# Kernel optimization log

Hardware: AMD Instinct MI355X
Metric: run time of the kernel (lower is better)

Reference implementation:

```python
import jax, jax.numpy as jnp
import numpy as np

B, L, D, H, N, F_, DM = 16, 2048, 128, 4, 4, 129, 16
DK = D // H
DFF = 2 * D
INT = int(np.sqrt(D))  # 11
V = F_ + 1


def _uinit(key, shape, fan):
    s = float(np.sqrt(6.0 / fan))
    return jax.random.uniform(key, shape, jnp.float32, -s, s)


def setup_inputs() -> dict:
    key = jax.random.key(0)
    ks = jax.random.split(key, 24)
    return {
        "values": jax.random.normal(ks[0], (B, L), jnp.float32),
        "times": jax.random.uniform(ks[1], (B, L), jnp.float32),
        "variables": jax.random.randint(ks[2], (B, L), 0, F_),
        "input_mask": jax.random.randint(ks[3], (B, L), 0, 2).astype(bool),
        "demographics": jax.random.normal(ks[4], (B, DM), jnp.float32),
        # CVE time
        "W1t": _uinit(ks[5], (1, INT), 1 + INT), "b1t": jnp.zeros((INT,), jnp.float32),
        "W2t": _uinit(ks[6], (INT, D), INT + D),
        # CVE value
        "W1v": _uinit(ks[7], (1, INT), 1 + INT), "b1v": jnp.zeros((INT,), jnp.float32),
        "W2v": _uinit(ks[8], (INT, D), INT + D),
        # variable embedding table
        "var_table": jax.random.normal(ks[9], (V, D), jnp.float32),
        # transformer stacks (init_proj: uniform(-s, s), s = sqrt(6/(fan_in+fan_out)) of last two dims)
        "Wq": _uinit(ks[10], (N, H, D, DK), D + DK),
        "Wk": _uinit(ks[11], (N, H, D, DK), D + DK),
        "Wv": _uinit(ks[12], (N, H, D, DK), D + DK),
        "Wo": _uinit(ks[13], (N, D, D), 2 * D),
        "W1": _uinit(ks[14], (N, D, DFF), D + DFF), "b1": jnp.zeros((N, 1, 1, DFF), jnp.float32),
        "W2": _uinit(ks[15], (N, DFF, D), DFF + D), "b2": jnp.zeros((N, 1, 1, D), jnp.float32),
        # fusion attention
        "Wf": _uinit(ks[16], (D, D), 2 * D), "bf": jnp.zeros((D,), jnp.float32),
        "uf": _uinit(ks[17], (D, 1), D + 1),
        # demographics MLP
        "Wd1": _uinit(ks[18], (DM, 2 * D), DM + 2 * D), "bd1": jnp.zeros((2 * D,), jnp.float32),
        "Wd2": _uinit(ks[19], (2 * D, D), 3 * D), "bd2": jnp.zeros((D,), jnp.float32),
        # head: forecast_fc
        "Wh": _uinit(ks[20], (2 * D, F_), 2 * D + F_), "bh": jnp.zeros((F_,), jnp.float32),
    }


def reference(values, times, variables, input_mask, demographics,
              W1t, b1t, W2t, W1v, b1v, W2v, var_table,
              Wq, Wk, Wv, Wo, W1, b1, W2, b2,
              Wf, bf, uf, Wd1, bd1, Wd2, bd2, Wh, bh):
    FMIN = jnp.finfo(values.dtype).min
    # demographics MLP
    demo = jnp.tanh(demographics @ Wd1 + bd1) @ Wd2 + bd2
    # continuous value embeddings (CVE): x -> tanh(x*W1 + b1) @ W2
    te = jnp.tanh(times[..., None] * W1t[0] + b1t) @ W2t    # [B,L,D]
    ve = jnp.tanh(values[..., None] * W1v[0] + b1v) @ W2v   # [B,L,D]
    x = te + ve + var_table[variables]                      # [B,L,D]
    # additive pairwise mask (finite FMIN, matches torch finfo.min semantics)
    m = input_mask
    pair = m[:, :, None] & m[:, None, :]                    # [B,L,L]
    addm = jnp.where(pair[:, None, :, :], 0.0, FMIN)        # [B,1,L,L]
    n_layers = Wq.shape[0]
    bsz, max_len, _ = x.shape
    for i in range(n_layers):
        q = jnp.einsum('bld,hde->bhle', x, Wq[i])
        k = jnp.einsum('bld,hde->bhle', x, Wk[i])
        v = jnp.einsum('bld,hde->bhle', x, Wv[i])
        A = jnp.einsum('bhle,bhke->bhlk', q, k) + addm      # NOTE: no 1/sqrt(dk) scaling, as in source
        A = jax.nn.softmax(A, axis=-1)
        o = jnp.einsum('bhlk,bhke->blhe', A, v).reshape(bsz, max_len, -1)
        x = o @ Wo[i] + x
        f = jax.nn.gelu(x @ W1[i] + b1[i], approximate=False)
        x = f @ W2[i] + b2[i] + x
    # fusion attention pooling
    att = (jnp.tanh(x @ Wf + bf) @ uf)[:, :, 0]             # [B,L]
    att = att + jnp.where(m, 0.0, FMIN)
    w = jax.nn.softmax(att, axis=-1)
    ts = jnp.sum(x * w[:, :, None], axis=1)                 # [B,D]
    emb = jnp.concatenate([ts, demo], axis=-1)              # [B,2D]
    return emb @ Wh + bh                                    # [B,features_num]
```

## Files before the change

kernel.cpp:

```cpp
#include <hip/hip_runtime.h>
#include <hip/hip_bf16.h>
#include <math.h>

#define B_   16
#define L_   2048
#define D_   128
#define H_   4
#define NL_  4
#define DK_  32
#define DFF_ 256
#define INTD_ 11
#define F_OUT 129
#define DM_  16
#define FMINV (-3.402823466e38f)
#define LOG2E 1.4426950408889634f

#define BL_  (B_*L_)
#define SZ_X (BL_*D_)

#define WT_Q 0
#define WT_K 16384
#define WT_V 32768
#define WT_O 49152
#define WT_1 65536
#define WT_2 98304
#define WT_TOT 131072

typedef __attribute__((ext_vector_type(8))) short bf16x8;
typedef __attribute__((ext_vector_type(4))) float f32x4;

#if __has_builtin(__builtin_amdgcn_exp2f)
#define EXP2F(x) __builtin_amdgcn_exp2f(x)
#else
#define EXP2F(x) __expf(0.69314718055994531f*(x))
#endif

static __device__ __forceinline__ short f2bf(float x) {
    union { __hip_bfloat16 h; short s; } u;
    u.h = __float2bfloat16(x);
    return u.s;
}
static __device__ __forceinline__ float bf2f(short s) {
    union { __hip_bfloat16 h; short t; } u;
    u.t = s;
    return __bfloat162float(u.h);
}
static __device__ __forceinline__ void split2(float v, short& h, short& l) {
    h = f2bf(v); l = f2bf(v - bf2f(h));
}
static __device__ __forceinline__ void split_trunc(float v, short& h, short& l) {
    unsigned u = __float_as_uint(v);
    h = (short)(u >> 16);
    float r = v - __uint_as_float(u & 0xffff0000u);
    l = (short)(__float_as_uint(r) >> 16);
}
static __device__ __forceinline__ void bar_lgkm() {
    asm volatile("s_waitcnt lgkmcnt(0)" ::: "memory");
    __builtin_amdgcn_s_barrier();
}
static __device__ __forceinline__ int find_b(const int* __restrict__ tp, int bidx) {
    int b = 0;
    while (bidx >= tp[b+1]) ++b;
    return b;
}

__global__ __launch_bounds__(256)
void compact_kernel(const int* __restrict__ mask, int* __restrict__ pos,
                    int* __restrict__ kcount, float* __restrict__ cfm,
                    float* __restrict__ x)
{
    int b = blockIdx.x, t = threadIdx.x;
    int lane = t & 63, w = t >> 6;
    __shared__ int wsum[4];
    __shared__ int tot_s;
    int mv[8], loc[8], s = 0;
#pragma unroll
    for (int i = 0; i < 8; ++i) {
        mv[i] = mask[b*L_ + t*8 + i];
        loc[i] = s;
        s += mv[i];
    }
    int v = s;
#pragma unroll
    for (int d = 1; d < 64; d <<= 1) {
        int y = __shfl_up(v, d);
        if (lane >= d) v += y;
    }
    int excl = v - s;
    if (lane == 63) wsum[w] = v;
    __syncthreads();
    int wbase = 0;
    for (int i = 0; i < w; ++i) wbase += wsum[i];
    int base = wbase + excl;
#pragma unroll
    for (int i = 0; i < 8; ++i)
        pos[b*L_ + t*8 + i] = mv[i] ? (base + loc[i]) : -1;
    if (t == 255) { kcount[b] = base + s; tot_s = base + s; }
    __syncthreads();
    int tot = tot_s;
    for (int l = t; l < L_; l += 256) cfm[b*L_ + l] = (l < tot) ? 0.0f : FMINV;
    int end = (tot + 63) & ~63;
    int nz = (end - tot) * D_;
    for (int i = t; i < nz; i += 256)
        x[((size_t)(b*2048 + tot))*D_ + i] = 0.0f;
}

__global__ __launch_bounds__(64)
void tile_prefix_kernel(const int* __restrict__ kcount, int* __restrict__ tprefix)
{
    if (threadIdx.x == 0) {
        int s = 0;
        for (int b = 0; b < B_; ++b) {
            tprefix[b] = s;
            s += (kcount[b] + 63) >> 6;
        }
        tprefix[B_] = s;
    }
}

__global__ __launch_bounds__(128)
void embed_kernel(const float* __restrict__ values, const float* __restrict__ times,
                  const int* __restrict__ variables, const int* __restrict__ pos,
                  const float* __restrict__ W1t, const float* __restrict__ b1t,
                  const float* __restrict__ W2t,
                  const float* __restrict__ W1v, const float* __restrict__ b1v,
                  const float* __restrict__ W2v,
                  const float* __restrict__ var_table, float* __restrict__ x)
{
    int bl = blockIdx.x;
    int p  = pos[bl];
    if (p < 0) return;
    int t  = threadIdx.x;
    __shared__ float th[INTD_], vh[INTD_];
    if (t < INTD_)                th[t]    = tanhf(times[bl]  * W1t[t]    + b1t[t]);
    if (t >= 64 && t < 64+INTD_)  vh[t-64] = tanhf(values[bl] * W1v[t-64] + b1v[t-64]);
    __syncthreads();
    int var = variables[bl];
    float acc = var_table[var*D_ + t];
#pragma unroll
    for (int i = 0; i < INTD_; ++i)
        acc += th[i]*W2t[i*D_ + t] + vh[i]*W2v[i*D_ + t];
    x[((size_t)((bl >> 11)*2048 + p))*D_ + t] = acc;
}

__global__ __launch_bounds__(256)
void split_all_kernel(const float* __restrict__ Wq, const float* __restrict__ Wk,
                      const float* __restrict__ Wv, const float* __restrict__ Wo,
                      const float* __restrict__ W1, const float* __restrict__ W2,
                      const float* __restrict__ Wf,
                      short* __restrict__ hi, short* __restrict__ lo)
{
    int gidx = blockIdx.x*256 + threadIdx.x;
    float v;
    if (gidx < NL_*131072) {
        int layer = gidx >> 17;
        int idx   = gidx & 131071;
        if (idx < 49152) {
            int which = idx >> 14;
            int r = idx & 16383;
            int col = r >> 7, k = r & 127;
            int h = col >> 5, e = col & 31;
            const float* src = ((which == 0) ? Wq : (which == 1) ? Wk : Wv)
                               + (size_t)layer*H_*D_*DK_;
            v = src[(h*D_ + k)*DK_ + e];
        } else if (idx < 65536) {
            int r = idx - 49152;
            int col = r >> 7, k = r & 127;
            v = Wo[(size_t)layer*D_*D_ + k*D_ + col];
        } else if (idx < 98304) {
            int r = idx - 65536;
            int col = r >> 7, k = r & 127;
            v = W1[(size_t)layer*D_*DFF_ + k*DFF_ + col];
        } else {
            int r = idx - 98304;
            int col = r >> 8, k = r & 255;
            v = W2[(size_t)layer*DFF_*D_ + k*D_ + col];
        }
    } else {
        int r = gidx - NL_*131072;
        int col = r >> 7, k = r & 127;
        v = Wf[k*D_ + col];
    }
    short h2, l2; split2(v, h2, l2);
    hi[gidx] = h2; lo[gidx] = l2;
}

__global__ __launch_bounds__(256)
void gemm_qkv_fused(const float* __restrict__ A, const short* __restrict__ Whi,
                    const short* __restrict__ Wlo, const int* __restrict__ tprefix,
                    float* __restrict__ qout,
                    short* __restrict__ khi, short* __restrict__ klo,
                    short* __restrict__ vhiT, short* __restrict__ vloT)
{
    const int bidx = blockIdx.x;
    if (bidx >= tprefix[B_]) return;
    const int bb = find_b(tprefix, bidx);
    const int row0 = bb*2048 + (bidx - tprefix[bb])*64;
    const int sec = blockIdx.y;

    __shared__ short Ahi[64*136];
    __shared__ short Alo[64*136];
    const int t = threadIdx.x;
    const int w = t >> 6, lane = t & 63;
    const int m = lane & 15, qd = lane >> 4;

#pragma unroll
    for (int i = 0; i < 8; ++i) {
        int r = (t >> 5) + 8*i;
        int c = (t & 31) * 4;
        float4 av = *(const float4*)(A + (size_t)(row0 + r)*D_ + c);
        short4 hi4, lo4;
        split2(av.x, hi4.x, lo4.x);
        split2(av.y, hi4.y, lo4.y);
        split2(av.z, hi4.z, lo4.z);
        split2(av.w, hi4.w, lo4.w);
        *(short4*)&Ahi[r*136 + c] = hi4;
        *(short4*)&Alo[r*136 + c] = lo4;
    }
    __syncthreads();

    const short* Wh = Whi + sec*16384;
    const short* Wl = Wlo + sec*16384;
    f32x4 acc[4][2];
#pragma unroll
    for (int r4 = 0; r4 < 4; ++r4)
#pragma unroll
        for (int j = 0; j < 2; ++j) acc[r4][j] = (f32x4){0,0,0,0};

#pragma unroll
    for (int ks = 0; ks < 4; ++ks) {
        bf16x8 wh[2], wl[2];
#pragma unroll
        for (int j = 0; j < 2; ++j) {
            size_t wi = (size_t)(32*w + 16*j + m)*D_ + 32*ks + 8*qd;
            wh[j] = *(const bf16x8*)(Wh + wi);
            wl[j] = *(const bf16x8*)(Wl + wi);
        }
#pragma unroll
        for (int r4 = 0; r4 < 4; ++r4) {
            bf16x8 ah = *(const bf16x8*)&Ahi[(16*r4 + m)*136 + 32*ks + 8*qd];
            bf16x8 al = *(const bf16x8*)&Alo[(16*r4 + m)*136 + 32*ks + 8*qd];
#pragma unroll
            for (int j = 0; j < 2; ++j) {
                acc[r4][j] = __builtin_amdgcn_mfma_f32_16x16x32_bf16(wh[j], ah, acc[r4][j], 0, 0, 0);
                acc[r4][j] = __builtin_amdgcn_mfma_f32_16x16x32_bf16(wh[j], al, acc[r4][j], 0, 0, 0);
                acc[r4][j] = __builtin_amdgcn_mfma_f32_16x16x32_bf16(wl[j], ah, acc[r4][j], 0, 0, 0);
            }
        }
    }

#pragma unroll
    for (int r4 = 0; r4 < 4; ++r4) {
        int row = row0 + 16*r4 + m;
        int l = row & 2047;
#pragma unroll
        for (int j = 0; j < 2; ++j) {
            int col = 32*w + 16*j + 4*qd;
            f32x4 v = acc[r4][j];
            if (sec == 0) {
                float4 sv = {v[0], v[1], v[2], v[3]};
                *(float4*)(qout + (size_t)row*D_ + col) = sv;
            } else if (sec == 1) {
                size_t idx = ((size_t)((bb*4 + w)*2048 + l))*32 + (col & 31);
                short4 hi4, lo4;
                split2(v[0], hi4.x, lo4.x);
                split2(v[1], hi4.y, lo4.y);
                split2(v[2], hi4.z, lo4.z);
                split2(v[3], hi4.w, lo4.w);
                *(short4*)(khi + idx) = hi4;
                *(short4*)(klo + idx) = lo4;
            } else {
                size_t basep = (size_t)(bb*4 + w)*32;
#pragma unroll
                for (int e = 0; e < 4; ++e) {
                    int d = 16*j + 4*qd + e;
                    short hh, ll; split2(v[e], hh, ll);
                    vhiT[(basep + d)*2048 + l] = hh;
                    vloT[(basep + d)*2048 + l] = ll;
                }
            }
        }
    }
}

__global__ __launch_bounds__(256)
void attn_mfma_kernel(const float* __restrict__ q,
                      const short* __restrict__ khi, const short* __restrict__ klo,
                      const short* __restrict__ vhiT, const short* __restrict__ vloT,
                      const int* __restrict__ kcount, const int* __restrict__ tprefix,
                      float* __restrict__ opart, float* __restrict__ mlm,
                      float* __restrict__ mll)
{
    __shared__ short KhiS[2][2048];
    __shared__ short KloS[2][2048];
    __shared__ short Vthi[2][2048];
    __shared__ short Vtlo[2][2048];
    __shared__ short Ps[4][1024];

    const int bidx = blockIdx.x;
    if (bidx >= tprefix[B_]) return;
    const int b  = find_b(tprefix, bidx);
    const int qt = bidx - tprefix[b];
    const int h = blockIdx.y & 3, half = blockIdx.y >> 2;

    const int t    = threadIdx.x;
    const int w    = t >> 6;
    const int lane = t & 63;
    const int m    = lane & 15;
    const int qd   = lane >> 4;

    const int Kb = kcount[b];
    const int nt = (Kb + 63) >> 6;
    const int ntH = (nt + 1) >> 1;
    const int kt0 = half * ntH;
    const int kt1 = (kt0 + ntH < nt) ? (kt0 + ntH) : nt;
    const size_t mlbase = (((size_t)(b*4 + h))*2 + half)*2048;

    if (kt0 >= kt1) {
        if (lane < 16) {
            mlm[mlbase + qt*64 + 16*w + lane] = FMINV;
            mll[mlbase + qt*64 + 16*w + lane] = 0.0f;
        }
        return;
    }

    const size_t hd = ((size_t)(b*4 + h))*2048*32;
    const int vd = t >> 3;
    const int vk = t & 7;
    const size_t vbase = ((size_t)(b*4 + h)*32 + vd)*2048 + vk*8;
    const int vw_off = vd*64 + ((vk ^ (vd & 7)) << 3);

    const int qrow = qt*64 + 16*w + m;
    const float* qp = q + ((size_t)(b*L_ + qrow))*D_ + h*DK_ + 8*qd;
    float qf[8];
    *(float4*)&qf[0] = *(const float4*)qp;
    *(float4*)&qf[4] = *(const float4*)(qp + 4);
    bf16x8 qhi, qlo;
#pragma unroll
    for (int j = 0; j < 8; ++j) {
        float qs = qf[j] * LOG2E;
        short hs = f2bf(qs);
        qhi[j] = hs;
        qlo[j] = f2bf(qs - bf2f(hs));
    }

    bf16x8 pkh, pkl, pvh, pvl;
    {
        const size_t gk = hd + (size_t)kt0*64*32 + t*8;
        pkh = *(const bf16x8*)(khi + gk);
        pkl = *(const bf16x8*)(klo + gk);
        pvh = *(const bf16x8*)(vhiT + vbase + (size_t)kt0*64);
        pvl = *(const bf16x8*)(vloT + vbase + (size_t)kt0*64);
    }

    float m_old = -INFINITY, l_run = 0.0f;
    f32x4 o_acc[2] = {{0,0,0,0},{0,0,0,0}};

    for (int kt = kt0; kt < kt1; ++kt) {
        const int buf = kt & 1;
        *(bf16x8*)&KhiS[buf][t*8] = pkh;
        *(bf16x8*)&KloS[buf][t*8] = pkl;
        *(bf16x8*)&Vthi[buf][vw_off] = pvh;
        *(bf16x8*)&Vtlo[buf][vw_off] = pvl;
        if (kt + 1 < kt1) {
            const size_t gk = hd + (size_t)(kt+1)*64*32 + t*8;
            pkh = *(const bf16x8*)(khi + gk);
            pkl = *(const bf16x8*)(klo + gk);
            pvh = *(const bf16x8*)(vhiT + vbase + (size_t)(kt+1)*64);
            pvl = *(const bf16x8*)(vloT + vbase + (size_t)(kt+1)*64);
        }
        bar_lgkm();
        __builtin_amdgcn_sched_barrier(0);

        f32x4 sf[4];
#pragma unroll
        for (int k4 = 0; k4 < 4; ++k4) {
            bf16x8 ka = *(const bf16x8*)&KhiS[buf][(16*k4 + m)*32 + 8*qd];
            bf16x8 kl = *(const bf16x8*)&KloS[buf][(16*k4 + m)*32 + 8*qd];
            f32x4 c = {0,0,0,0};
            c = __builtin_amdgcn_mfma_f32_16x16x32_bf16(ka, qhi, c, 0, 0, 0);
            c = __builtin_amdgcn_mfma_f32_16x16x32_bf16(ka, qlo, c, 0, 0, 0);
            c = __builtin_amdgcn_mfma_f32_16x16x32_bf16(kl, qhi, c, 0, 0, 0);
            sf[k4] = c;
        }

        float sv[16];
        if (kt == nt - 1) {
            const int rel = Kb - kt*64;
#pragma unroll
            for (int k4 = 0; k4 < 4; ++k4)
#pragma unroll
                for (int e = 0; e < 4; ++e)
                    sv[4*k4+e] = sf[k4][e] +
                        (((16*k4 + 4*qd + e) < rel) ? 0.0f : FMINV);
        } else {
#pragma unroll
            for (int k4 = 0; k4 < 4; ++k4)
#pragma unroll
                for (int e = 0; e < 4; ++e)
                    sv[4*k4+e] = sf[k4][e];
        }

        float mx8[8];
#pragma unroll
        for (int j = 0; j < 8; ++j) mx8[j] = fmaxf(sv[2*j], sv[2*j+1]);
#pragma unroll
        for (int j = 0; j < 4; ++j) mx8[j] = fmaxf(mx8[j], mx8[j+4]);
        float tmax = fmaxf(fmaxf(mx8[0], mx8[1]), fmaxf(mx8[2], mx8[3]));
        tmax = fmaxf(tmax, __shfl_xor(tmax, 16));
        tmax = fmaxf(tmax, __shfl_xor(tmax, 32));
        float mnew  = fmaxf(m_old, tmax);
        float alpha = EXP2F(m_old - mnew);
        float pj[16];
        short pbh[16], pbl[16];
#pragma unroll
        for (int j = 0; j < 16; ++j) {
            float p = EXP2F(sv[j] - mnew);
            pj[j] = p;
            split_trunc(p, pbh[j], pbl[j]);
        }
        float ps8[8];
#pragma unroll
        for (int j = 0; j < 8; ++j) ps8[j] = pj[2*j] + pj[2*j+1];
#pragma unroll
        for (int j = 0; j < 4; ++j) ps8[j] = ps8[j] + ps8[j+4];
        float psum = (ps8[0] + ps8[1]) + (ps8[2] + ps8[3]);
        psum += __shfl_xor(psum, 16);
        psum += __shfl_xor(psum, 32);
        l_run = l_run * alpha + psum;
        m_old = mnew;

#pragma unroll
        for (int k4 = 0; k4 < 4; ++k4) {
            short4 s4h;
            s4h.x = pbh[4*k4+0]; s4h.y = pbh[4*k4+1]; s4h.z = pbh[4*k4+2]; s4h.w = pbh[4*k4+3];
            int chunk = 2*k4 + (qd >> 1);
            int po = m*64 + ((chunk ^ (m & 7)) << 3) + ((qd & 1) << 2);
            *(short4*)&Ps[w][po] = s4h;
        }

        {
            float a0 = __shfl(alpha, 4*qd + 0);
            float a1 = __shfl(alpha, 4*qd + 1);
            float a2 = __shfl(alpha, 4*qd + 2);
            float a3 = __shfl(alpha, 4*qd + 3);
            o_acc[0][0]*=a0; o_acc[0][1]*=a1; o_acc[0][2]*=a2; o_acc[0][3]*=a3;
            o_acc[1][0]*=a0; o_acc[1][1]*=a1; o_acc[1][2]*=a2; o_acc[1][3]*=a3;
        }
#pragma unroll
        for (int s = 0; s < 2; ++s) {
#pragma unroll
            for (int tp = 0; tp < 2; ++tp) {
                bf16x8 pah = *(const bf16x8*)&Ps[w][m*64 + (((4*s + qd) ^ (m & 7)) << 3)];
                int vr = (16*tp + m)*64 + (((4*s + qd) ^ (m & 7)) << 3);
                bf16x8 vh = *(const bf16x8*)&Vthi[buf][vr];
                bf16x8 vl = *(const bf16x8*)&Vtlo[buf][vr];
                o_acc[tp] = __builtin_amdgcn_mfma_f32_16x16x32_bf16(pah, vh, o_acc[tp], 0, 0, 0);
                o_acc[tp] = __builtin_amdgcn_mfma_f32_16x16x32_bf16(pah, vl, o_acc[tp], 0, 0, 0);
            }
        }
#pragma unroll
        for (int k4 = 0; k4 < 4; ++k4) {
            short4 s4l;
            s4l.x = pbl[4*k4+0]; s4l.y = pbl[4*k4+1]; s4l.z = pbl[4*k4+2]; s4l.w = pbl[4*k4+3];
            int chunk = 2*k4 + (qd >> 1);
            int po = m*64 + ((chunk ^ (m & 7)) << 3) + ((qd & 1) << 2);
            *(short4*)&Ps[w][po] = s4l;
        }
#pragma unroll
        for (int s = 0; s < 2; ++s) {
#pragma unroll
            for (int tp = 0; tp < 2; ++tp) {
                bf16x8 pal = *(const bf16x8*)&Ps[w][m*64 + (((4*s + qd) ^ (m & 7)) << 3)];
                int vr = (16*tp + m)*64 + (((4*s + qd) ^ (m & 7)) << 3);
                bf16x8 vh = *(const bf16x8*)&Vthi[buf][vr];
                o_acc[tp] = __builtin_amdgcn_mfma_f32_16x16x32_bf16(pal, vh, o_acc[tp], 0, 0, 0);
            }
        }
    }

    if (lane < 16) {
        mlm[mlbase + qt*64 + 16*w + lane] = m_old;
        mll[mlbase + qt*64 + 16*w + lane] = l_run;
    }
    float* ob = opart + (size_t)half*SZ_X;
#pragma unroll
    for (int tp = 0; tp < 2; ++tp)
#pragma unroll
        for (int r = 0; r < 4; ++r)
            ob[((size_t)(b*L_ + qt*64 + 16*w + 4*qd + r))*D_ + h*DK_ + 16*tp + m] =
                o_acc[tp][r];
}

__global__ __launch_bounds__(256)
void wo_ffn1_kernel(const float* __restrict__ opart, const float* __restrict__ mlm,
                    const float* __restrict__ mll,
                    const short* __restrict__ WhiO, const short* __restrict__ WloO,
                    const short* __restrict__ Whi1, const short* __restrict__ Wlo1,
                    const float* __restrict__ b1,
                    const int* __restrict__ tprefix, float* __restrict__ x,
                    float* __restrict__ hb)
{
    const int bidx = blockIdx.x;
    if (bidx >= tprefix[B_]) return;
    const int bb = find_b(tprefix, bidx);
    const int row0 = bb*2048 + (bidx - tprefix[bb])*64;

    __shared__ short Ahi[64*136];
    __shared__ short Alo[64*136];
    const int t = threadIdx.x;
    const int w = t >> 6, lane = t & 63;
    const int m = lane & 15, qd = lane >> 4;

#pragma unroll
    for (int i = 0; i < 8; ++i) {
        int r = (t >> 5) + 8*i;
        int c = (t & 31) * 4;
        int row = row0 + r;
        int l = row & 2047;
        int h = c >> 5;
        size_t i0 = (((size_t)(bb*4 + h))*2 + 0)*2048 + l;
        size_t i1 = i0 + 2048;
        float m0 = mlm[i0], m1 = mlm[i1];
        float l0 = mll[i0], l1 = mll[i1];
        float M  = fmaxf(m0, m1);
        float w0 = EXP2F(m0 - M), w1 = EXP2F(m1 - M);
        float inv = 1.0f / (l0*w0 + l1*w1);
        float s0 = w0 * inv, s1 = w1 * inv;
        float4 o0 = *(const float4*)(opart + (size_t)row*D_ + c);
        float4 o1 = *(const float4*)(opart + (size_t)(BL_ + row)*D_ + c);
        float4 av;
        av.x = s0*o0.x + s1*o1.x;
        av.y = s0*o0.y + s1*o1.y;
        av.z = s0*o0.z + s1*o1.z;
        av.w = s0*o0.w + s1*o1.w;
        short4 hi4, lo4;
        split2(av.x, hi4.x, lo4.x);
        split2(av.y, hi4.y, lo4.y);
        split2(av.z, hi4.z, lo4.z);
        split2(av.w, hi4.w, lo4.w);
        *(short4*)&Ahi[r*136 + c] = hi4;
        *(short4*)&Alo[r*136 + c] = lo4;
    }
    __syncthreads();

    f32x4 acc[4][2];
#pragma unroll
    for (int r4 = 0; r4 < 4; ++r4)
#pragma unroll
        for (int j = 0; j < 2; ++j) acc[r4][j] = (f32x4){0,0,0,0};
#pragma unroll
    for (int ks = 0; ks < 4; ++ks) {
        bf16x8 wh[2], wl[2];
#pragma unroll
        for (int j = 0; j < 2; ++j) {
            size_t wi = (size_t)(32*w + 16*j + m)*D_ + 32*ks + 8*qd;
            wh[j] = *(const bf16x8*)(WhiO + wi);
            wl[j] = *(const bf16x8*)(WloO + wi);
        }
#pragma unroll
        for (int r4 = 0; r4 < 4; ++r4) {
            bf16x8 ah = *(const bf16x8*)&Ahi[(16*r4 + m)*136 + 32*ks + 8*qd];
            bf16x8 al = *(const bf16x8*)&Alo[(16*r4 + m)*136 + 32*ks + 8*qd];
#pragma unroll
            for (int j = 0; j < 2; ++j) {
                acc[r4][j] = __builtin_amdgcn_mfma_f32_16x16x32_bf16(wh[j], ah, acc[r4][j], 0, 0, 0);
                acc[r4][j] = __builtin_amdgcn_mfma_f32_16x16x32_bf16(wh[j], al, acc[r4][j], 0, 0, 0);
                acc[r4][j] = __builtin_amdgcn_mfma_f32_16x16x32_bf16(wl[j], ah, acc[r4][j], 0, 0, 0);
            }
        }
    }

#pragma unroll
    for (int r4 = 0; r4 < 4; ++r4) {
        int row = row0 + 16*r4 + m;
#pragma unroll
        for (int j = 0; j < 2; ++j) {
            int col = 32*w + 16*j + 4*qd;
            float4 rv = *(const float4*)(x + (size_t)row*D_ + col);
            acc[r4][j][0] += rv.x; acc[r4][j][1] += rv.y;
            acc[r4][j][2] += rv.z; acc[r4][j][3] += rv.w;
            float4 sv = {acc[r4][j][0], acc[r4][j][1], acc[r4][j][2], acc[r4][j][3]};
            *(float4*)(x + (size_t)row*D_ + col) = sv;
        }
    }
    __syncthreads();

#pragma unroll
    for (int r4 = 0; r4 < 4; ++r4) {
#pragma unroll
        for (int j = 0; j < 2; ++j) {
            int col = 32*w + 16*j + 4*qd;
            short4 hi4, lo4;
            split2(acc[r4][j][0], hi4.x, lo4.x);
            split2(acc[r4][j][1], hi4.y, lo4.y);
            split2(acc[r4][j][2], hi4.z, lo4.z);
            split2(acc[r4][j][3], hi4.w, lo4.w);
            *(short4*)&Ahi[(16*r4 + m)*136 + col] = hi4;
            *(short4*)&Alo[(16*r4 + m)*136 + col] = lo4;
        }
    }
    __syncthreads();

    f32x4 a2[4][4];
#pragma unroll
    for (int r4 = 0; r4 < 4; ++r4)
#pragma unroll
        for (int jj = 0; jj < 4; ++jj) a2[r4][jj] = (f32x4){0,0,0,0};
#pragma unroll
    for (int ks = 0; ks < 4; ++ks) {
        bf16x8 wh[4], wl[4];
#pragma unroll
        for (int jj = 0; jj < 4; ++jj) {
            size_t wi = (size_t)(64*w + 16*jj + m)*D_ + 32*ks + 8*qd;
            wh[jj] = *(const bf16x8*)(Whi1 + wi);
            wl[jj] = *(const bf16x8*)(Wlo1 + wi);
        }
#pragma unroll
        for (int r4 = 0; r4 < 4; ++r4) {
            bf16x8 ah = *(const bf16x8*)&Ahi[(16*r4 + m)*136 + 32*ks + 8*qd];
            bf16x8 al = *(const bf16x8*)&Alo[(16*r4 + m)*136 + 32*ks + 8*qd];
#pragma unroll
            for (int jj = 0; jj < 4; ++jj) {
                a2[r4][jj] = __builtin_amdgcn_mfma_f32_16x16x32_bf16(wh[jj], ah, a2[r4][jj], 0, 0, 0);
                a2[r4][jj] = __builtin_amdgcn_mfma_f32_16x16x32_bf16(wh[jj], al, a2[r4][jj], 0, 0, 0);
                a2[r4][jj] = __builtin_amdgcn_mfma_f32_16x16x32_bf16(wl[jj], ah, a2[r4][jj], 0, 0, 0);
            }
        }
    }

#pragma unroll
    for (int r4 = 0; r4 < 4; ++r4) {
        int row = row0 + 16*r4 + m;
#pragma unroll
        for (int jj = 0; jj < 4; ++jj) {
            int col = 64*w + 16*jj + 4*qd;
            f32x4 v = a2[r4][jj];
            float4 bv = *(const float4*)(b1 + col);
            v[0] += bv.x; v[1] += bv.y; v[2] += bv.z; v[3] += bv.w;
#pragma unroll
            for (int e = 0; e < 4; ++e)
                v[e] = 0.5f * v[e] * (1.0f + erff(v[e] * 0.70710678118654752f));
            float4 sv = {v[0], v[1], v[2], v[3]};
            *(float4*)(hb + (size_t)row*DFF_ + col) = sv;
        }
    }
}

template<int TAIL>
__global__ __launch_bounds__(256)
void ffn2_next_kernel(const float* __restrict__ hb,
                      const short* __restrict__ Whi2, const short* __restrict__ Wlo2,
                      const float* __restrict__ b2,
                      const short* __restrict__ WhiN, const short* __restrict__ WloN,
                      const float* __restrict__ bfv, const float* __restrict__ uf,
                      const float* __restrict__ cfm,
                      const int* __restrict__ tprefix, float* __restrict__ x,
                      float* __restrict__ qout,
                      short* __restrict__ khi, short* __restrict__ klo,
                      short* __restrict__ vhiT, short* __restrict__ vloT,
                      float* __restrict__ attb)
{
    const int bidx = blockIdx.x;
    if (bidx >= tprefix[B_]) return;
    const int bb = find_b(tprefix, bidx);
    const int row0 = bb*2048 + (bidx - tprefix[bb])*64;

    __shared__ short Ahi[64*136];
    __shared__ short Alo[64*136];
    __shared__ float part[64][16];
    const int t = threadIdx.x;
    const int w = t >> 6, lane = t & 63;
    const int m = lane & 15, qd = lane >> 4;

    f32x4 acc[4][2];
#pragma unroll
    for (int r4 = 0; r4 < 4; ++r4)
#pragma unroll
        for (int j = 0; j < 2; ++j) acc[r4][j] = (f32x4){0,0,0,0};

    for (int kb = 0; kb < DFF_; kb += 128) {
        if (kb) __syncthreads();
#pragma unroll
        for (int i = 0; i < 8; ++i) {
            int r = (t >> 5) + 8*i;
            int c = (t & 31) * 4;
            float4 av = *(const float4*)(hb + (size_t)(row0 + r)*DFF_ + kb + c);
            short4 hi4, lo4;
            split2(av.x, hi4.x, lo4.x);
            split2(av.y, hi4.y, lo4.y);
            split2(av.z, hi4.z, lo4.z);
            split2(av.w, hi4.w, lo4.w);
            *(short4*)&Ahi[r*136 + c] = hi4;
            *(short4*)&Alo[r*136 + c] = lo4;
        }
        __syncthreads();

#pragma unroll
        for (int ks = 0; ks < 4; ++ks) {
            bf16x8 wh[2], wl[2];
#pragma unroll
            for (int j = 0; j < 2; ++j) {
                size_t wi = (size_t)(32*w + 16*j + m)*DFF_ + kb + 32*ks + 8*qd;
                wh[j] = *(const bf16x8*)(Whi2 + wi);
                wl[j] = *(const bf16x8*)(Wlo2 + wi);
            }
#pragma unroll
            for (int r4 = 0; r4 < 4; ++r4) {
                bf16x8 ah = *(const bf16x8*)&Ahi[(16*r4 + m)*136 + 32*ks + 8*qd];
                bf16x8 al = *(const bf16x8*)&Alo[(16*r4 + m)*136 + 32*ks + 8*qd];
#pragma unroll
                for (int j = 0; j < 2; ++j) {
                    acc[r4][j] = __builtin_amdgcn_mfma_f32_16x16x32_bf16(wh[j], ah, acc[r4][j], 0, 0, 0);
                    acc[r4][j] = __builtin_amdgcn_mfma_f32_16x16x32_bf16(wh[j], al, acc[r4][j], 0, 0, 0);
                    acc[r4][j] = __builtin_amdgcn_mfma_f32_16x16x32_bf16(wl[j], ah, acc[r4][j], 0, 0, 0);
                }
            }
        }
    }

#pragma unroll
    for (int r4 = 0; r4 < 4; ++r4) {
        int row = row0 + 16*r4 + m;
#pragma unroll
        for (int j = 0; j < 2; ++j) {
            int col = 32*w + 16*j + 4*qd;
            float4 bv = *(const float4*)(b2 + col);
            float4 rv = *(const float4*)(x + (size_t)row*D_ + col);
            acc[r4][j][0] += bv.x + rv.x; acc[r4][j][1] += bv.y + rv.y;
            acc[r4][j][2] += bv.z + rv.z; acc[r4][j][3] += bv.w + rv.w;
            float4 sv = {acc[r4][j][0], acc[r4][j][1], acc[r4][j][2], acc[r4][j][3]};
            *(float4*)(x + (size_t)row*D_ + col) = sv;
        }
    }
    __syncthreads();

#pragma unroll
    for (int r4 = 0; r4 < 4; ++r4) {
#pragma unroll
        for (int j = 0; j < 2; ++j) {
            int col = 32*w + 16*j + 4*qd;
            short4 hi4, lo4;
            split2(acc[r4][j][0], hi4.x, lo4.x);
            split2(acc[r4][j][1], hi4.y, lo4.y);
            split2(acc[r4][j][2], hi4.z, lo4.z);
            split2(acc[r4][j][3], hi4.w, lo4.w);
            *(short4*)&Ahi[(16*r4 + m)*136 + col] = hi4;
            *(short4*)&Alo[(16*r4 + m)*136 + col] = lo4;
        }
    }
    __syncthreads();

    if (TAIL == 0) {
#pragma unroll
        for (int sec = 0; sec < 3; ++sec) {
            const short* Wh = WhiN + sec*16384;
            const short* Wl = WloN + sec*16384;
            f32x4 a3[4][2];
#pragma unroll
            for (int r4 = 0; r4 < 4; ++r4)
#pragma unroll
                for (int j = 0; j < 2; ++j) a3[r4][j] = (f32x4){0,0,0,0};
#pragma unroll
            for (int ks = 0; ks < 4; ++ks) {
                bf16x8 wh[2], wl[2];
#pragma unroll
                for (int j = 0; j < 2; ++j) {
                    size_t wi = (size_t)(32*w + 16*j + m)*D_ + 32*ks + 8*qd;
                    wh[j] = *(const bf16x8*)(Wh + wi);
                    wl[j] = *(const bf16x8*)(Wl + wi);
                }
#pragma unroll
                for (int r4 = 0; r4 < 4; ++r4) {
                    bf16x8 ah = *(const bf16x8*)&Ahi[(16*r4 + m)*136 + 32*ks + 8*qd];
                    bf16x8 al = *(const bf16x8*)&Alo[(16*r4 + m)*136 + 32*ks + 8*qd];
#pragma unroll
                    for (int j = 0; j < 2; ++j) {
                        a3[r4][j] = __builtin_amdgcn_mfma_f32_16x16x32_bf16(wh[j], ah, a3[r4][j], 0, 0, 0);
                        a3[r4][j] = __builtin_amdgcn_mfma_f32_16x16x32_bf16(wh[j], al, a3[r4][j], 0, 0, 0);
                        a3[r4][j] = __builtin_amdgcn_mfma_f32_16x16x32_bf16(wl[j], ah, a3[r4][j], 0, 0, 0);
                    }
                }
            }
#pragma unroll
            for (int r4 = 0; r4 < 4; ++r4) {
                int row = row0 + 16*r4 + m;
                int l = row & 2047;
#pragma unroll
                for (int j = 0; j < 2; ++j) {
                    int col = 32*w + 16*j + 4*qd;
                    f32x4 v = a3[r4][j];
                    if (sec == 0) {
                        float4 sv = {v[0], v[1], v[2], v[3]};
                        *(float4*)(qout + (size_t)row*D_ + col) = sv;
                    } else if (sec == 1) {
                        size_t idx = ((size_t)((bb*4 + w)*2048 + l))*32 + (col & 31);
                        short4 hi4, lo4;
                        split2(v[0], hi4.x, lo4.x);
                        split2(v[1], hi4.y, lo4.y);
                        split2(v[2], hi4.z, lo4.z);
                        split2(v[3], hi4.w, lo4.w);
                        *(short4*)(khi + idx) = hi4;
                        *(short4*)(klo + idx) = lo4;
                    } else {
                        size_t basep = (size_t)(bb*4 + w)*32;
#pragma unroll
                        for (int e = 0; e < 4; ++e) {
                            int d = 16*j + 4*qd + e;
                            short hh, ll; split2(v[e], hh, ll);
                            vhiT[(basep + d)*2048 + l] = hh;
                            vloT[(basep + d)*2048 + l] = ll;
                        }
                    }
                }
            }
        }
    } else {
        f32x4 a3[4][2];
#pragma unroll
        for (int r4 = 0; r4 < 4; ++r4)
#pragma unroll
            for (int j = 0; j < 2; ++j) a3[r4][j] = (f32x4){0,0,0,0};
#pragma unroll
        for (int ks = 0; ks < 4; ++ks) {
            bf16x8 wh[2], wl[2];
#pragma unroll
            for (int j = 0; j < 2; ++j) {
                size_t wi = (size_t)(32*w + 16*j + m)*D_ + 32*ks + 8*qd;
                wh[j] = *(const bf16x8*)(WhiN + wi);
                wl[j] = *(const bf16x8*)(WloN + wi);
            }
#pragma unroll
            for (int r4 = 0; r4 < 4; ++r4) {
                bf16x8 ah = *(const bf16x8*)&Ahi[(16*r4 + m)*136 + 32*ks + 8*qd];
                bf16x8 al = *(const bf16x8*)&Alo[(16*r4 + m)*136 + 32*ks + 8*qd];
#pragma unroll
                for (int j = 0; j < 2; ++j) {
                    a3[r4][j] = __builtin_amdgcn_mfma_f32_16x16x32_bf16(wh[j], ah, a3[r4][j], 0, 0, 0);
                    a3[r4][j] = __builtin_amdgcn_mfma_f32_16x16x32_bf16(wh[j], al, a3[r4][j], 0, 0, 0);
                    a3[r4][j] = __builtin_amdgcn_mfma_f32_16x16x32_bf16(wl[j], ah, a3[r4][j], 0, 0, 0);
                }
            }
        }
#pragma unroll
        for (int r4 = 0; r4 < 4; ++r4) {
            float dotp = 0.0f;
#pragma unroll
            for (int j = 0; j < 2; ++j) {
                int col = 32*w + 16*j + 4*qd;
                f32x4 v = a3[r4][j];
                float4 bv = *(const float4*)(bfv + col);
                v[0] += bv.x; v[1] += bv.y; v[2] += bv.z; v[3] += bv.w;
#pragma unroll
                for (int e = 0; e < 4; ++e) v[e] = tanhf(v[e]);
                float4 uv = *(const float4*)(uf + col);
                dotp += v[0]*uv.x + v[1]*uv.y + v[2]*uv.z + v[3]*uv.w;
            }
            part[16*r4 + m][4*w + qd] = dotp;
        }
        __syncthreads();
        if (t < 64) {
            float s = 0.0f;
#pragma unroll
            for (int i = 0; i < 16; ++i) s += part[t][i];
            attb[row0 + t] = s + cfm[row0 + t];
        }
    }
}

__global__ __launch_bounds__(256)
void pool_stats_kernel(const float* __restrict__ att, const int* __restrict__ kcount,
                       float* __restrict__ p)
{
    int b = blockIdx.x, t = threadIdx.x;
    int lim = (kcount[b] + 63) & ~63;
    __shared__ float red[4];
    __shared__ float a_s[L_];

    float m = -INFINITY;
    for (int l = t; l < L_; l += 256) {
        float a = (l < lim) ? att[b*L_ + l] : FMINV;
        a_s[l] = a;
        m = fmaxf(m, a);
    }
#pragma unroll
    for (int s = 1; s < 64; s <<= 1) m = fmaxf(m, __shfl_xor(m, s));
    if ((t & 63) == 0) red[t >> 6] = m;
    __syncthreads();
    m = fmaxf(fmaxf(red[0], red[1]), fmaxf(red[2], red[3]));
    __syncthreads();

    float s = 0.0f;
    for (int l = t; l < L_; l += 256) s += __expf(a_s[l] - m);
#pragma unroll
    for (int st = 1; st < 64; st <<= 1) s += __shfl_xor(s, st);
    if ((t & 63) == 0) red[t >> 6] = s;
    __syncthreads();
    s = red[0] + red[1] + red[2] + red[3];
    float inv = 1.0f / s;
    for (int l = t; l < L_; l += 256)
        p[b*L_ + l] = (l < lim) ? __expf(a_s[l] - m) * inv : 0.0f;
}

__global__ __launch_bounds__(128)
void pool_partial_kernel(const float* __restrict__ p, const float* __restrict__ x,
                         float* __restrict__ part)
{
    int c = blockIdx.x, b = blockIdx.y, d = threadIdx.x;
    const float* xb = x + ((size_t)(b*L_ + c*128))*D_ + d;
    const float* pb = p + b*L_ + c*128;
    float acc = 0.0f;
#pragma unroll 4
    for (int i = 0; i < 128; ++i) acc += pb[i] * xb[(size_t)i*D_];
    part[((size_t)b*16 + c)*D_ + d] = acc;
}

__global__ __launch_bounds__(256)
void head_kernel(const float* __restrict__ part, const float* __restrict__ demog,
                 const float* __restrict__ Wd1, const float* __restrict__ bd1,
                 const float* __restrict__ Wd2, const float* __restrict__ bd2,
                 const float* __restrict__ Wh, const float* __restrict__ bh,
                 float* __restrict__ out)
{
    int b = blockIdx.x, t = threadIdx.x;
    __shared__ float tss[128];
    __shared__ float hs1[256];
    __shared__ float dems[128];
    if (t < 128) {
        float s = 0.0f;
#pragma unroll
        for (int c = 0; c < 16; ++c) s += part[((size_t)b*16 + c)*D_ + t];
        tss[t] = s;
    }
    {
        float a = bd1[t];
#pragma unroll
        for (int kk = 0; kk < DM_; ++kk) a += demog[b*DM_ + kk] * Wd1[kk*(2*D_) + t];
        hs1[t] = tanhf(a);
    }
    __syncthreads();
    if (t < 128) {
        float a = bd2[t];
        for (int kk = 0; kk < 2*D_; ++kk) a += hs1[kk] * Wd2[kk*D_ + t];
        dems[t] = a;
    }
    __syncthreads();
    if (t >= F_OUT) return;
    float acc = bh[t];
    for (int k2 = 0; k2 < D_; ++k2) acc += tss[k2]  * Wh[k2*F_OUT + t];
    for (int k2 = 0; k2 < D_; ++k2) acc += dems[k2] * Wh[(D_+k2)*F_OUT + t];
    out[b*F_OUT + t] = acc;
}

extern "C" void kernel_launch(void* const* d_in, const int* in_sizes, int n_in,
                              void* d_out, int out_size, void* d_ws, size_t ws_size,
                              hipStream_t stream)
{
    (void)in_sizes; (void)n_in; (void)out_size; (void)ws_size;
    const float* values       = (const float*)d_in[0];
    const float* times        = (const float*)d_in[1];
    const int*   variables    = (const int*)  d_in[2];
    const int*   input_mask   = (const int*)  d_in[3];
    const float* demographics = (const float*)d_in[4];
    const float* W1t = (const float*)d_in[5];
    const float* b1t = (const float*)d_in[6];
    const float* W2t = (const float*)d_in[7];
    const float* W1v = (const float*)d_in[8];
    const float* b1v = (const float*)d_in[9];
    const float* W2v = (const float*)d_in[10];
    const float* var_table = (const float*)d_in[11];
    const float* Wq  = (const float*)d_in[12];
    const float* Wk  = (const float*)d_in[13];
    const float* Wv  = (const float*)d_in[14];
    const float* Wo  = (const float*)d_in[15];
    const float* W1  = (const float*)d_in[16];
    const float* b1  = (const float*)d_in[17];
    const float* W2  = (const float*)d_in[18];
    const float* b2  = (const float*)d_in[19];
    const float* Wf  = (const float*)d_in[20];
    const float* bfv = (const float*)d_in[21];
    const float* uf  = (const float*)d_in[22];
    const float* Wd1 = (const float*)d_in[23];
    const float* bd1 = (const float*)d_in[24];
    const float* Wd2 = (const float*)d_in[25];
    const float* bd2 = (const float*)d_in[26];
    const float* Wh  = (const float*)d_in[27];
    const float* bhv = (const float*)d_in[28];
    float* out = (float*)d_out;

    float* ws     = (float*)d_ws;
    float* x      = ws;
    float* qb     = ws + (size_t)SZ_X;
    float* region = ws + (size_t)2*SZ_X;
    short* khi    = (short*)region;
    short* klo    = khi + (size_t)SZ_X;
    short* vhiT   = klo + (size_t)SZ_X;
    short* vloT   = vhiT + (size_t)SZ_X;
    float* attb   = ws + (size_t)4*SZ_X;
    float* attp   = attb + BL_;
    float* partb  = attp + BL_;
    short* wt_hi  = (short*)(partb + B_*16*D_);
    short* wt_lo  = wt_hi + ((size_t)NL_*WT_TOT + 16384);
    int*   posb   = (int*)(wt_lo + ((size_t)NL_*WT_TOT + 16384));
    int*   kcountb= posb + BL_;
    int*   tprefb = kcountb + B_;
    float* cfmb   = (float*)(kcountb + 40);
    float* opart  = cfmb + BL_;
    float* mlm    = opart + (size_t)2*SZ_X;
    float* mll    = mlm + (size_t)B_*H_*2*2048;
    float* hb     = mll + (size_t)B_*H_*2*2048;
    short* wfhi   = wt_hi + (size_t)NL_*WT_TOT;
    short* wflo   = wt_lo + (size_t)NL_*WT_TOT;

    compact_kernel<<<B_, 256, 0, stream>>>(input_mask, posb, kcountb, cfmb, x);
    tile_prefix_kernel<<<1, 64, 0, stream>>>(kcountb, tprefb);
    embed_kernel<<<BL_, 128, 0, stream>>>(values, times, variables, posb,
                                          W1t, b1t, W2t, W1v, b1v, W2v,
                                          var_table, x);
    split_all_kernel<<<(NL_*131072 + 16384)/256, 256, 0, stream>>>(
        Wq, Wk, Wv, Wo, W1, W2, Wf, wt_hi, wt_lo);

    gemm_qkv_fused<<<dim3(512, 3), 256, 0, stream>>>(x,
        wt_hi + 0*WT_TOT, wt_lo + 0*WT_TOT, tprefb, qb, khi, klo, vhiT, vloT);

    for (int i = 0; i < NL_; ++i) {
        short* whL = wt_hi + (size_t)i*WT_TOT;
        short* wlL = wt_lo + (size_t)i*WT_TOT;
        attn_mfma_kernel<<<dim3(512, H_*2), 256, 0, stream>>>(qb, khi, klo,
            vhiT, vloT, kcountb, tprefb, opart, mlm, mll);
        wo_ffn1_kernel<<<512, 256, 0, stream>>>(opart, mlm, mll,
            whL+WT_O, wlL+WT_O, whL+WT_1, wlL+WT_1, b1 + i*DFF_,
            tprefb, x, hb);
        if (i < NL_ - 1) {
            short* whN = wt_hi + (size_t)(i+1)*WT_TOT;
            short* wlN = wt_lo + (size_t)(i+1)*WT_TOT;
            ffn2_next_kernel<0><<<512, 256, 0, stream>>>(hb,
                whL+WT_2, wlL+WT_2, b2 + i*D_, whN, wlN,
                nullptr, nullptr, nullptr, tprefb, x,
                qb, khi, klo, vhiT, vloT, nullptr);
        } else {
            ffn2_next_kernel<1><<<512, 256, 0, stream>>>(hb,
                whL+WT_2, wlL+WT_2, b2 + i*D_, wfhi, wflo,
                bfv, uf, cfmb, tprefb, x,
                nullptr, nullptr, nullptr, nullptr, nullptr, attb);
        }
    }

    pool_stats_kernel<<<B_, 256, 0, stream>>>(attb, kcountb, attp);
    pool_partial_kernel<<<dim3(16, B_), 128, 0, stream>>>(attp, x, partb);
    head_kernel<<<B_, 256, 0, stream>>>(partb, demographics, Wd1, bd1, Wd2, bd2,
                                        Wh, bhv, out);
}
```

Measured before the change: 649.2 us.

## Split FFN1 and next-layer QKV projections across extra grid dimension with redundant recompute

The Wo+FFN1 kernel now launches two blocks per row tile, each computing half of the FFN1 output columns. Both halves redundantly recompute the Wo projection, and only one writes the residual into a new xmid buffer. The FFN2+next-QKV kernel launches three blocks per tile, one per Q/K/V section, each redundantly recomputing FFN2. The goal is more parallelism and lower per-block register pressure, paid for with duplicated GEMM work and an extra residual buffer that avoids read/write races on x.

```diff
diff --git a/kernel.cpp b/kernel.cpp
--- a/kernel.cpp
+++ b/kernel.cpp
@@ -498,13 +498,14 @@
                     const short* __restrict__ WhiO, const short* __restrict__ WloO,
                     const short* __restrict__ Whi1, const short* __restrict__ Wlo1,
                     const float* __restrict__ b1,
-                    const int* __restrict__ tprefix, float* __restrict__ x,
-                    float* __restrict__ hb)
+                    const int* __restrict__ tprefix, const float* __restrict__ x,
+                    float* __restrict__ xmid, float* __restrict__ hb)
 {
     const int bidx = blockIdx.x;
     if (bidx >= tprefix[B_]) return;
     const int bb = find_b(tprefix, bidx);
     const int row0 = bb*2048 + (bidx - tprefix[bb])*64;
+    const int nh = blockIdx.y;
 
     __shared__ short Ahi[64*136];
     __shared__ short Alo[64*136];
@@ -580,8 +581,10 @@
             float4 rv = *(const float4*)(x + (size_t)row*D_ + col);
             acc[r4][j][0] += rv.x; acc[r4][j][1] += rv.y;
             acc[r4][j][2] += rv.z; acc[r4][j][3] += rv.w;
-            float4 sv = {acc[r4][j][0], acc[r4][j][1], acc[r4][j][2], acc[r4][j][3]};
-            *(float4*)(x + (size_t)row*D_ + col) = sv;
+            if (nh == 0) {
+                float4 sv = {acc[r4][j][0], acc[r4][j][1], acc[r4][j][2], acc[r4][j][3]};
+                *(float4*)(xmid + (size_t)row*D_ + col) = sv;
+            }
         }
     }
     __syncthreads();
@@ -602,17 +605,17 @@
     }
     __syncthreads();
 
-    f32x4 a2[4][4];
+    f32x4 a2[4][2];
 #pragma unroll
     for (int r4 = 0; r4 < 4; ++r4)
 #pragma unroll
-        for (int jj = 0; jj < 4; ++jj) a2[r4][jj] = (f32x4){0,0,0,0};
+        for (int jj = 0; jj < 2; ++jj) a2[r4][jj] = (f32x4){0,0,0,0};
 #pragma unroll
     for (int ks = 0; ks < 4; ++ks) {
-        bf16x8 wh[4], wl[4];
-#pragma unroll
-        for (int jj = 0; jj < 4; ++jj) {
-            size_t wi = (size_t)(64*w + 16*jj + m)*D_ + 32*ks + 8*qd;
+        bf16x8 wh[2], wl[2];
+#pragma unroll
+        for (int jj = 0; jj < 2; ++jj) {
+            size_t wi = (size_t)(128*nh + 32*w + 16*jj + m)*D_ + 32*ks + 8*qd;
             wh[jj] = *(const bf16x8*)(Whi1 + wi);
             wl[jj] = *(const bf16x8*)(Wlo1 + wi);
         }
@@ -621,7 +624,7 @@
             bf16x8 ah = *(const bf16x8*)&Ahi[(16*r4 + m)*136 + 32*ks + 8*qd];
             bf16x8 al = *(const bf16x8*)&Alo[(16*r4 + m)*136 + 32*ks + 8*qd];
 #pragma unroll
-            for (int jj = 0; jj < 4; ++jj) {
+            for (int jj = 0; jj < 2; ++jj) {
                 a2[r4][jj] = __builtin_amdgcn_mfma_f32_16x16x32_bf16(wh[jj], ah, a2[r4][jj], 0, 0, 0);
                 a2[r4][jj] = __builtin_amdgcn_mfma_f32_16x16x32_bf16(wh[jj], al, a2[r4][jj], 0, 0, 0);
                 a2[r4][jj] = __builtin_amdgcn_mfma_f32_16x16x32_bf16(wl[jj], ah, a2[r4][jj], 0, 0, 0);
@@ -633,8 +636,8 @@
     for (int r4 = 0; r4 < 4; ++r4) {
         int row = row0 + 16*r4 + m;
 #pragma unroll
-        for (int jj = 0; jj < 4; ++jj) {
-            int col = 64*w + 16*jj + 4*qd;
+        for (int jj = 0; jj < 2; ++jj) {
+            int col = 128*nh + 32*w + 16*jj + 4*qd;
             f32x4 v = a2[r4][jj];
             float4 bv = *(const float4*)(b1 + col);
             v[0] += bv.x; v[1] += bv.y; v[2] += bv.z; v[3] += bv.w;
@@ -655,7 +658,8 @@
                       const short* __restrict__ WhiN, const short* __restrict__ WloN,
                       const float* __restrict__ bfv, const float* __restrict__ uf,
                       const float* __restrict__ cfm,
-                      const int* __restrict__ tprefix, float* __restrict__ x,
+                      const int* __restrict__ tprefix, const float* __restrict__ xmid,
+                      float* __restrict__ x,
                       float* __restrict__ qout,
                       short* __restrict__ khi, short* __restrict__ klo,
                       short* __restrict__ vhiT, short* __restrict__ vloT,
@@ -665,6 +669,7 @@
     if (bidx >= tprefix[B_]) return;
     const int bb = find_b(tprefix, bidx);
     const int row0 = bb*2048 + (bidx - tprefix[bb])*64;
+    const int sec = blockIdx.y;
 
     __shared__ short Ahi[64*136];
     __shared__ short Alo[64*136];
@@ -726,11 +731,13 @@
         for (int j = 0; j < 2; ++j) {
             int col = 32*w + 16*j + 4*qd;
             float4 bv = *(const float4*)(b2 + col);
-            float4 rv = *(const float4*)(x + (size_t)row*D_ + col);
+            float4 rv = *(const float4*)(xmid + (size_t)row*D_ + col);
             acc[r4][j][0] += bv.x + rv.x; acc[r4][j][1] += bv.y + rv.y;
             acc[r4][j][2] += bv.z + rv.z; acc[r4][j][3] += bv.w + rv.w;
-            float4 sv = {acc[r4][j][0], acc[r4][j][1], acc[r4][j][2], acc[r4][j][3]};
-            *(float4*)(x + (size_t)row*D_ + col) = sv;
+            if (TAIL == 1 || sec == 0) {
+                float4 sv = {acc[r4][j][0], acc[r4][j][1], acc[r4][j][2], acc[r4][j][3]};
+                *(float4*)(x + (size_t)row*D_ + col) = sv;
+            }
         }
     }
     __syncthreads();
@@ -752,65 +759,62 @@
     __syncthreads();
 
     if (TAIL == 0) {
-#pragma unroll
-        for (int sec = 0; sec < 3; ++sec) {
-            const short* Wh = WhiN + sec*16384;
-            const short* Wl = WloN + sec*16384;
-            f32x4 a3[4][2];
-#pragma unroll
-            for (int r4 = 0; r4 < 4; ++r4)
-#pragma unroll
-                for (int j = 0; j < 2; ++j) a3[r4][j] = (f32x4){0,0,0,0};
-#pragma unroll
-            for (int ks = 0; ks < 4; ++ks) {
-                bf16x8 wh[2], wl[2];
+        const short* Wh = WhiN + sec*16384;
+        const short* Wl = WloN + sec*16384;
+        f32x4 a3[4][2];
+#pragma unroll
+        for (int r4 = 0; r4 < 4; ++r4)
+#pragma unroll
+            for (int j = 0; j < 2; ++j) a3[r4][j] = (f32x4){0,0,0,0};
+#pragma unroll
+        for (int ks = 0; ks < 4; ++ks) {
+            bf16x8 wh[2], wl[2];
+#pragma unroll
+            for (int j = 0; j < 2; ++j) {
+                size_t wi = (size_t)(32*w + 16*j + m)*D_ + 32*ks + 8*qd;
+                wh[j] = *(const bf16x8*)(Wh + wi);
+                wl[j] = *(const bf16x8*)(Wl + wi);
+            }
+#pragma unroll
+            for (int r4 = 0; r4 < 4; ++r4) {
+                bf16x8 ah = *(const bf16x8*)&Ahi[(16*r4 + m)*136 + 32*ks + 8*qd];
+                bf16x8 al = *(const bf16x8*)&Alo[(16*r4 + m)*136 + 32*ks + 8*qd];
 #pragma unroll
                 for (int j = 0; j < 2; ++j) {
-                    size_t wi = (size_t)(32*w + 16*j + m)*D_ + 32*ks + 8*qd;
-                    wh[j] = *(const bf16x8*)(Wh + wi);
-                    wl[j] = *(const bf16x8*)(Wl + wi);
+                    a3[r4][j] = __builtin_amdgcn_mfma_f32_16x16x32_bf16(wh[j], ah, a3[r4][j], 0, 0, 0);
+                    a3[r4][j] = __builtin_amdgcn_mfma_f32_16x16x32_bf16(wh[j], al, a3[r4][j], 0, 0, 0);
+                    a3[r4][j] = __builtin_amdgcn_mfma_f32_16x16x32_bf16(wl[j], ah, a3[r4][j], 0, 0, 0);
                 }
-#pragma unroll
-                for (int r4 = 0; r4 < 4; ++r4) {
-                    bf16x8 ah = *(const bf16x8*)&Ahi[(16*r4 + m)*136 + 32*ks + 8*qd];
-                    bf16x8 al = *(const bf16x8*)&Alo[(16*r4 + m)*136 + 32*ks + 8*qd];
-#pragma unroll
-                    for (int j = 0; j < 2; ++j) {
-                        a3[r4][j] = __builtin_amdgcn_mfma_f32_16x16x32_bf16(wh[j], ah, a3[r4][j], 0, 0, 0);
-                        a3[r4][j] = __builtin_amdgcn_mfma_f32_16x16x32_bf16(wh[j], al, a3[r4][j], 0, 0, 0);
-                        a3[r4][j] = __builtin_amdgcn_mfma_f32_16x16x32_bf16(wl[j], ah, a3[r4][j], 0, 0, 0);
-                    }
-                }
-            }
-#pragma unroll
-            for (int r4 = 0; r4 < 4; ++r4) {
-                int row = row0 + 16*r4 + m;
-                int l = row & 2047;
-#pragma unroll
-                for (int j = 0; j < 2; ++j) {
-                    int col = 32*w + 16*j + 4*qd;
-                    f32x4 v = a3[r4][j];
-                    if (sec == 0) {
-                        float4 sv = {v[0], v[1], v[2], v[3]};
-                        *(float4*)(qout + (size_t)row*D_ + col) = sv;
-                    } else if (sec == 1) {
-                        size_t idx = ((size_t)((bb*4 + w)*2048 + l))*32 + (col & 31);
-                        short4 hi4, lo4;
-                        split2(v[0], hi4.x, lo4.x);
-                        split2(v[1], hi4.y, lo4.y);
-                        split2(v[2], hi4.z, lo4.z);
-                        split2(v[3], hi4.w, lo4.w);
-                        *(short4*)(khi + idx) = hi4;
-                        *(short4*)(klo + idx) = lo4;
-                    } else {
-                        size_t basep = (size_t)(bb*4 + w)*32;
-#pragma unroll
-                        for (int e = 0; e < 4; ++e) {
-                            int d = 16*j + 4*qd + e;
-                            short hh, ll; split2(v[e], hh, ll);
-                            vhiT[(basep + d)*2048 + l] = hh;
-                            vloT[(basep + d)*2048 + l] = ll;
-                        }
+            }
+        }
+#pragma unroll
+        for (int r4 = 0; r4 < 4; ++r4) {
+            int row = row0 + 16*r4 + m;
+            int l = row & 2047;
+#pragma unroll
+            for (int j = 0; j < 2; ++j) {
+                int col = 32*w + 16*j + 4*qd;
+                f32x4 v = a3[r4][j];
+                if (sec == 0) {
+                    float4 sv = {v[0], v[1], v[2], v[3]};
+                    *(float4*)(qout + (size_t)row*D_ + col) = sv;
+                } else if (sec == 1) {
+                    size_t idx = ((size_t)((bb*4 + w)*2048 + l))*32 + (col & 31);
+                    short4 hi4, lo4;
+                    split2(v[0], hi4.x, lo4.x);
+                    split2(v[1], hi4.y, lo4.y);
+                    split2(v[2], hi4.z, lo4.z);
+                    split2(v[3], hi4.w, lo4.w);
+                    *(short4*)(khi + idx) = hi4;
+                    *(short4*)(klo + idx) = lo4;
+                } else {
+                    size_t basep = (size_t)(bb*4 + w)*32;
+#pragma unroll
+                    for (int e = 0; e < 4; ++e) {
+                        int d = 16*j + 4*qd + e;
+                        short hh, ll; split2(v[e], hh, ll);
+                        vhiT[(basep + d)*2048 + l] = hh;
+                        vloT[(basep + d)*2048 + l] = ll;
                     }
                 }
             }
@@ -1009,6 +1013,7 @@
     float* mlm    = opart + (size_t)2*SZ_X;
     float* mll    = mlm + (size_t)B_*H_*2*2048;
     float* hb     = mll + (size_t)B_*H_*2*2048;
+    float* xmid   = hb + (size_t)2*SZ_X;
     short* wfhi   = wt_hi + (size_t)NL_*WT_TOT;
     short* wflo   = wt_lo + (size_t)NL_*WT_TOT;
 
@@ -1028,20 +1033,20 @@
         short* wlL = wt_lo + (size_t)i*WT_TOT;
         attn_mfma_kernel<<<dim3(512, H_*2), 256, 0, stream>>>(qb, khi, klo,
             vhiT, vloT, kcountb, tprefb, opart, mlm, mll);
-        wo_ffn1_kernel<<<512, 256, 0, stream>>>(opart, mlm, mll,
+        wo_ffn1_kernel<<<dim3(512, 2), 256, 0, stream>>>(opart, mlm, mll,
             whL+WT_O, wlL+WT_O, whL+WT_1, wlL+WT_1, b1 + i*DFF_,
-            tprefb, x, hb);
+            tprefb, x, xmid, hb);
         if (i < NL_ - 1) {
             short* whN = wt_hi + (size_t)(i+1)*WT_TOT;
             short* wlN = wt_lo + (size_t)(i+1)*WT_TOT;
-            ffn2_next_kernel<0><<<512, 256, 0, stream>>>(hb,
+            ffn2_next_kernel<0><<<dim3(512, 3), 256, 0, stream>>>(hb,
                 whL+WT_2, wlL+WT_2, b2 + i*D_, whN, wlN,
-                nullptr, nullptr, nullptr, tprefb, x,
+                nullptr, nullptr, nullptr, tprefb, xmid, x,
                 qb, khi, klo, vhiT, vloT, nullptr);
         } else {
             ffn2_next_kernel<1><<<512, 256, 0, stream>>>(hb,
                 whL+WT_2, wlL+WT_2, b2 + i*D_, wfhi, wflo,
-                bfv, uf, cfmb, tprefb, x,
+                bfv, uf, cfmb, tprefb, xmid, x,
                 nullptr, nullptr, nullptr, nullptr, nullptr, attb);
         }
     }
```

Result: no change. 648.5 us (-0.1%).
